# Kernel optimization log

Measured on AMD Instinct MI355X. Metric: run time of the kernel, lower is better.

Reference implementation:

```python
import jax, jax.numpy as jnp
import numpy as np

B = 4096          # number of graphs
NPG = 148         # nodes per graph (fixed by ReadOut(num_nodes=148))
N = B * NPG       # total nodes = 606208
EPG = 592         # edges per graph (~avg degree 4: RNA backbone + base pairs)
E = B * EPG       # total edges = 2424832


def setup_inputs() -> dict:
    key = jax.random.key(0)
    ks = jax.random.split(key, 10)
    x = jax.random.normal(ks[0], (N, 4), jnp.float32)
    # edges confined within each graph via per-graph node offsets
    src = jax.random.randint(ks[1], (E,), 0, NPG, dtype=jnp.int32)
    dst = jax.random.randint(ks[2], (E,), 0, NPG, dtype=jnp.int32)
    offs = jnp.repeat(jnp.arange(B, dtype=jnp.int32) * NPG, EPG)
    edge_index = jnp.stack([src + offs, dst + offs], axis=0)
    batch = jnp.repeat(jnp.arange(B, dtype=jnp.int32), NPG)
    # GCNConv weights (glorot-ish) and biases: 4->16->32->64
    def glorot(k, fi, fo):
        return jax.random.normal(k, (fi, fo), jnp.float32) * np.sqrt(2.0 / (fi + fo)).astype(np.float32)
    W1 = glorot(ks[3], 4, 16); b1 = jnp.zeros((16,), jnp.float32)
    W2 = glorot(ks[4], 16, 32); b2 = jnp.zeros((32,), jnp.float32)
    W3 = glorot(ks[5], 32, 64); b3 = jnp.zeros((64,), jnp.float32)
    return {"x": x, "edge_index": edge_index, "batch": batch,
            "W1": W1, "b1": b1, "W2": W2, "b2": b2, "W3": W3, "b3": b3}


def gcn_conv(x, src, dst, W, b, n):
    """PyG GCNConv: x' = D^{-1/2}(A+I)D^{-1/2} (x W) + b."""
    h = x @ W                                   # [n, out]
    loop = jnp.arange(n, dtype=src.dtype)       # self loops
    s = jnp.concatenate([src, loop])
    d = jnp.concatenate([dst, loop])
    deg = jax.ops.segment_sum(jnp.ones_like(s, h.dtype), d, num_segments=n)
    dis = jnp.where(deg > 0, jax.lax.rsqrt(jnp.maximum(deg, 1e-12)), 0.0)
    norm = dis[s] * dis[d]                      # [n_edges_with_loops]
    msg = h[s] * norm[:, None]                  # gather + normalize
    return jax.ops.segment_sum(msg, d, num_segments=n) + b


def reference(x, edge_index, batch, W1, b1, W2, b2, W3, b3):
    src, dst = edge_index[0], edge_index[1]
    n = x.shape[0]
    # Dropout(p=0.1) is identity at inference time
    h = jax.nn.relu(gcn_conv(x, src, dst, W1, b1, n))
    h = jax.nn.relu(gcn_conv(h, src, dst, W2, b2, n))
    h = jax.nn.relu(gcn_conv(h, src, dst, W3, b3, n))
    # to_dense_batch with max_num_nodes=148: every graph has exactly 148 nodes
    # and `batch` is sorted block-constant, so dense batching == reshape.
    dense = h.reshape(B, NPG, h.shape[-1])      # [B, 148, 64]
    return dense.reshape(B, -1)                 # Flatten -> [B, 9472]
```

## Files before the change

### kernel.cpp

```cpp
#include <hip/hip_runtime.h>

#define NPG 148
#define EPG 592
#define NTHR 256
#define SA   40
#define MT   10

typedef _Float16 h8 __attribute__((ext_vector_type(8)));
typedef _Float16 h4 __attribute__((ext_vector_type(4)));
typedef float    f4 __attribute__((ext_vector_type(4)));

__device__ __forceinline__ float f16bits_to_f32(unsigned short u) {
    return (float)__builtin_bit_cast(_Float16, u);
}


template<int Fi, int Fo, int KC, int NTN, int MAXJ, int WROW, int BOFF, bool LAST>
__device__ __forceinline__ void layer(int t,
    _Float16* __restrict__ A16, const _Float16* __restrict__ Wt,
    const _Float16* __restrict__ s_bh, const unsigned int* __restrict__ s_csr,
    const unsigned short* __restrict__ s_row, const unsigned short* __restrict__ s_dis,
    float* __restrict__ gout)
{
    float a[KC][8];
    if (t < NPG) {
        const float dd = f16bits_to_f32(s_dis[t]);
        const char* selfb = reinterpret_cast<const char*>(A16) + t * (SA * 2);
        #pragma unroll
        for (int kc = 0; kc < KC; ++kc) {
            const h8 hv = *reinterpret_cast<const h8*>(selfb + kc * 16);
            #pragma unroll
            for (int u = 0; u < 8; ++u) a[kc][u] = dd * (float)hv[u];
        }
        int e  = s_row[t];
        const int e1 = s_row[t + 1];
        unsigned int pk = (e < e1) ? s_csr[e] : 0u;
        while (e < e1) {
            const unsigned int pknext = (e + 1 < e1) ? s_csr[e + 1] : 0u;
            const char* mb = reinterpret_cast<const char*>(A16) + (pk & 0xffffu);
            const float ds = f16bits_to_f32((unsigned short)(pk >> 16));
            #pragma unroll
            for (int kc = 0; kc < KC; ++kc) {
                const h8 m = *reinterpret_cast<const h8*>(mb + kc * 16);
                #pragma unroll
                for (int u = 0; u < 8; ++u) a[kc][u] = fmaf((float)m[u], ds, a[kc][u]);
            }
            pk = pknext;
            ++e;
        }
        #pragma unroll
        for (int kc = 0; kc < KC; ++kc)
            #pragma unroll
            for (int u = 0; u < 8; ++u) a[kc][u] *= dd;
    }
    __syncthreads();
    if (t < NPG) {
        char* selfb = reinterpret_cast<char*>(A16) + t * (SA * 2);
        #pragma unroll
        for (int kc = 0; kc < KC; ++kc) {
            h8 pv;
            #pragma unroll
            for (int u = 0; u < 8; ++u) pv[u] = (_Float16)a[kc][u];
            *reinterpret_cast<h8*>(selfb + kc * 16) = pv;
        }
    }
    __syncthreads();

    const int w   = t >> 6;
    const int l16 = t & 15;
    const int q   = (t >> 4) & 3;
    h8 af[MAXJ], bf[MAXJ];
    #pragma unroll
    for (int j = 0; j < MAXJ; ++j) {
        const int idx = w + 4 * j;
        if (idx < MT * NTN) {
            const int mt = idx / NTN, nt = idx % NTN;
            af[j] = *reinterpret_cast<const h8*>(&A16[(mt * 16 + l16) * SA + q * 8]);
            bf[j] = *reinterpret_cast<const h8*>(&Wt[(WROW + nt * 16 + l16) * SA + q * 8]);
        }
    }
    __syncthreads();
    #pragma unroll
    for (int j = 0; j < MAXJ; ++j) {
        const int idx = w + 4 * j;
        if (idx < MT * NTN) {
            const int mt = idx / NTN, nt = idx % NTN;
            f4 acc = {0.f, 0.f, 0.f, 0.f};
            acc = __builtin_amdgcn_mfma_f32_16x16x32_f16(af[j], bf[j], acc, 0, 0, 0);
            const int col  = nt * 16 + l16;
            const float bias = (float)s_bh[BOFF + col];
            #pragma unroll
            for (int rr = 0; rr < 4; ++rr) {
                const float v = fmaxf(acc[rr] + bias, 0.f);
                const int row = mt * 16 + q * 4 + rr;
                if (LAST) {
                    if (row < NPG) gout[row * 64 + col] = v;
                } else {
                    A16[row * SA + col] = (_Float16)v;
                }
            }
        }
    }
    if (!LAST) __syncthreads();
}

__global__ __launch_bounds__(256, 6)
void gcn_fused(const float* __restrict__ x,
               const int* __restrict__ esrc, const int* __restrict__ edst,
               const float* __restrict__ W1, const float* __restrict__ b1,
               const float* __restrict__ W2, const float* __restrict__ b2,
               const float* __restrict__ W3, const float* __restrict__ b3,
               float* __restrict__ out)
{
    __shared__ __align__(16) _Float16 A16[160 * SA];
    __shared__ __align__(16) _Float16 Wt[112 * SA];
    __shared__ _Float16 s_bh[112];
    __shared__ unsigned int s_csr[EPG];
    __shared__ unsigned short s_row[152];
    __shared__ unsigned short s_dis[NPG];
    __shared__ int s_cnt[NPG], s_cnt2[NPG];

    int* s_edge = reinterpret_cast<int*>(Wt);

    const int t  = threadIdx.x;
    const int g  = blockIdx.x;
    const int be = g * EPG;
    const int bn = g * NPG;

    if (t < NPG) { s_cnt[t] = 0; s_cnt2[t] = 0; }
    for (int e = t; e < EPG; e += NTHR) {
        const int s = esrc[be + e] - bn;
        const int d = edst[be + e] - bn;
        s_edge[e] = s | (d << 8);
    }
    __syncthreads();

    for (int e = t; e < EPG; e += NTHR)
        atomicAdd(&s_cnt[((unsigned)s_edge[e]) >> 8], 1);
    __syncthreads();

    if (t < NPG) {
        const float disf = rsqrtf((float)(s_cnt[t] + 1));
        s_dis[t] = __builtin_bit_cast(unsigned short, (_Float16)disf);
    }
    if (t < 64) {
        const int lane = t;
        int v0 = s_cnt[lane];
        int v1 = s_cnt[64 + lane];
        int v2 = (128 + lane < NPG) ? s_cnt[128 + lane] : 0;
        #pragma unroll
        for (int off = 1; off < 64; off <<= 1) {
            const int u0 = __shfl_up(v0, off);
            const int u1 = __shfl_up(v1, off);
            const int u2 = __shfl_up(v2, off);
            if (lane >= off) { v0 += u0; v1 += u1; v2 += u2; }
        }
        const int t0 = __shfl(v0, 63);
        const int t1 = __shfl(v1, 63);
        v1 += t0;
        v2 += t0 + t1;
        if (lane == 0) s_row[0] = 0;
        s_row[1 + lane]  = (unsigned short)v0;
        s_row[65 + lane] = (unsigned short)v1;
        if (128 + lane < NPG) s_row[129 + lane] = (unsigned short)v2;
    }
    __syncthreads();

    for (int e = t; e < EPG; e += NTHR) {
        const int pk = s_edge[e];
        const int s  = pk & 0xFF;
        const int d  = (unsigned)pk >> 8;
        const int pos = (int)s_row[d] + atomicAdd(&s_cnt2[d], 1);
        s_csr[pos] = (unsigned int)(s * (SA * 2)) | ((unsigned int)s_dis[s] << 16);
    }
    __syncthreads();

    for (int i = t; i < 160 * SA / 8; i += NTHR) reinterpret_cast<f4*>(A16)[i] = f4{0.f, 0.f, 0.f, 0.f};
    for (int i = t; i < 112 * SA / 8; i += NTHR) reinterpret_cast<f4*>(Wt)[i]  = f4{0.f, 0.f, 0.f, 0.f};
    __syncthreads();
    for (int i = t; i < 64;   i += NTHR) Wt[(i & 15) * SA + (i >> 4)]        = (_Float16)W1[i];
    for (int i = t; i < 512;  i += NTHR) Wt[(16 + (i & 31)) * SA + (i >> 5)] = (_Float16)W2[i];
    for (int i = t; i < 2048; i += NTHR) Wt[(48 + (i & 63)) * SA + (i >> 6)] = (_Float16)W3[i];
    if (t < 16)       s_bh[t] = (_Float16)b1[t];
    else if (t < 48)  s_bh[t] = (_Float16)b2[t - 16];
    else if (t < 112) s_bh[t] = (_Float16)b3[t - 48];
    if (t < NPG) {
        const float4 xv = reinterpret_cast<const float4*>(x)[bn + t];
        h4 p; p[0] = (_Float16)xv.x; p[1] = (_Float16)xv.y; p[2] = (_Float16)xv.z; p[3] = (_Float16)xv.w;
        *reinterpret_cast<h4*>(&A16[t * SA]) = p;
    }
    __syncthreads();

    float* gout = out + (size_t)bn * 64;
    layer< 4, 16,  1,  1,   3,    0,   0, false>(t, A16, Wt, s_bh, s_csr, s_row, s_dis, gout);
    layer<16, 32,  2,  2,   5,   16,  16, false>(t, A16, Wt, s_bh, s_csr, s_row, s_dis, gout);
    layer<32, 64,  4,  4,  10,   48,  48, true >(t, A16, Wt, s_bh, s_csr, s_row, s_dis, gout);
}

extern "C" void kernel_launch(void* const* d_in, const int* in_sizes, int n_in,
                              void* d_out, int out_size, void* d_ws, size_t ws_size,
                              hipStream_t stream)
{
    const float* x  = (const float*)d_in[0];
    const int*   ei = (const int*)d_in[1];
    const float* W1 = (const float*)d_in[3];
    const float* b1 = (const float*)d_in[4];
    const float* W2 = (const float*)d_in[5];
    const float* b2 = (const float*)d_in[6];
    const float* W3 = (const float*)d_in[7];
    const float* b3 = (const float*)d_in[8];
    float* out = (float*)d_out;

    const int N = in_sizes[0] / 4;
    const int B = N / NPG;
    const int E = in_sizes[1] / 2;

    gcn_fused<<<B, NTHR, 0, stream>>>(x, ei, ei + E, W1, b1, W2, b2, W3, b3, out);
}
```

Before: 64.96 us.

## Split per-graph CSR construction into a separate setup kernel via workspace

Moves degree counting, the prefix scan, the normalization factors and the CSR edge sort out of the fused kernel into a new setup kernel. The setup kernel handles one graph per wavefront and writes packed CSR entries and row/degree metadata to the workspace. The main kernel then just loads the precomputed CSR and metadata into LDS, which shortens its serial prologue and cuts its LDS use, aiming at higher occupancy. It also shrinks the activation row stride from 40 to 36 halves, with a separate 40-half stride for weights, and vectorizes the W3 load. The trade-offs are an extra launch and an extra global write and read of the CSR data, and the 72-byte activation rows leave the 16-byte LDS vector loads only 8-byte aligned.

```diff
diff --git a/kernel.cpp b/kernel.cpp
--- a/kernel.cpp
+++ b/kernel.cpp
@@ -3,28 +3,120 @@
 #define NPG 148
 #define EPG 592
 #define NTHR 256
-#define SA   40
+#define SA   36
+#define SW   40
 #define MT   10
+#define MPG  149
 
 typedef _Float16 h8 __attribute__((ext_vector_type(8)));
 typedef _Float16 h4 __attribute__((ext_vector_type(4)));
 typedef float    f4 __attribute__((ext_vector_type(4)));
-
-__device__ __forceinline__ float f16bits_to_f32(unsigned short u) {
+typedef unsigned int u32;
+
+__device__ __forceinline__ float f16b(unsigned short u) {
     return (float)__builtin_bit_cast(_Float16, u);
 }
-
+__device__ __forceinline__ u32 f16u(float v) {
+    return (u32)__builtin_bit_cast(unsigned short, (_Float16)v);
+}
+
+__global__ __launch_bounds__(256, 8)
+void gcn_setup(const int* __restrict__ esrc, const int* __restrict__ edst,
+               u32* __restrict__ csr_g, u32* __restrict__ meta_g)
+{
+    __shared__ int cnt[4][160];
+    __shared__ u32 rows[4][148];
+    __shared__ u32 cbuf[4][EPG];
+
+    const int t  = threadIdx.x;
+    const int wv = t >> 6;
+    const int l  = t & 63;
+    const int g  = blockIdx.x * 4 + wv;
+    const int be = g * EPG;
+    const int bn = g * NPG;
+
+    u32 ep[10];
+    #pragma unroll
+    for (int k = 0; k < 10; ++k) {
+        const int e = l + k * 64;
+        ep[k] = 0xffffffffu;
+        if (e < EPG) {
+            const int s = esrc[be + e] - bn;
+            const int d = edst[be + e] - bn;
+            ep[k] = (u32)(s | (d << 8));
+        }
+    }
+    cnt[wv][l] = 0; cnt[wv][64 + l] = 0;
+    if (l < 32) cnt[wv][128 + l] = 0;
+    __syncthreads();
+
+    #pragma unroll
+    for (int k = 0; k < 10; ++k)
+        if (ep[k] != 0xffffffffu) atomicAdd(&cnt[wv][(ep[k] >> 8) & 0xff], 1);
+    __syncthreads();
+
+    const int c0 = cnt[wv][l];
+    const int c1 = cnt[wv][64 + l];
+    const int c2 = (l < 20) ? cnt[wv][128 + l] : 0;
+    int v0 = c0, v1 = c1, v2 = c2;
+    #pragma unroll
+    for (int off = 1; off < 64; off <<= 1) {
+        const int u0 = __shfl_up(v0, off);
+        const int u1 = __shfl_up(v1, off);
+        const int u2 = __shfl_up(v2, off);
+        if (l >= off) { v0 += u0; v1 += u1; v2 += u2; }
+    }
+    const int t0 = __shfl(v0, 63);
+    const int t1 = __shfl(v1, 63);
+    const int r0 = v0 - c0;
+    const int r1 = v1 - c1 + t0;
+    const int r2 = v2 - c2 + t0 + t1;
+    const u32 m0 = ((u32)r0 << 16) | f16u(rsqrtf((float)(c0 + 1)));
+    const u32 m1 = ((u32)r1 << 16) | f16u(rsqrtf((float)(c1 + 1)));
+    const u32 m2 = ((u32)r2 << 16) | f16u(rsqrtf((float)(c2 + 1)));
+    rows[wv][l] = m0;
+    rows[wv][64 + l] = m1;
+    if (l < 20) rows[wv][128 + l] = m2;
+    const size_t gm = (size_t)g * MPG;
+    meta_g[gm + l] = m0;
+    meta_g[gm + 64 + l] = m1;
+    if (l < 20) meta_g[gm + 128 + l] = m2;
+    if (l == 0) meta_g[gm + 148] = (u32)EPG << 16;
+
+    __syncthreads();
+    cnt[wv][l] = 0; cnt[wv][64 + l] = 0;
+    if (l < 32) cnt[wv][128 + l] = 0;
+    __syncthreads();
+
+    #pragma unroll
+    for (int k = 0; k < 10; ++k)
+        if (ep[k] != 0xffffffffu) {
+            const int s = ep[k] & 0xff;
+            const int d = (ep[k] >> 8) & 0xff;
+            const int pos = (int)(rows[wv][d] >> 16) + atomicAdd(&cnt[wv][d], 1);
+            cbuf[wv][pos] = (u32)(s * (SA * 2)) | ((rows[wv][s] & 0xffffu) << 16);
+        }
+    __syncthreads();
+
+    u32* cg = csr_g + (size_t)g * EPG;
+    #pragma unroll
+    for (int k = 0; k < 10; ++k) {
+        const int e = l + k * 64;
+        if (e < EPG) cg[e] = cbuf[wv][e];
+    }
+}
 
 template<int Fi, int Fo, int KC, int NTN, int MAXJ, int WROW, int BOFF, bool LAST>
 __device__ __forceinline__ void layer(int t,
     _Float16* __restrict__ A16, const _Float16* __restrict__ Wt,
-    const _Float16* __restrict__ s_bh, const unsigned int* __restrict__ s_csr,
-    const unsigned short* __restrict__ s_row, const unsigned short* __restrict__ s_dis,
-    float* __restrict__ gout)
+    const _Float16* __restrict__ s_bh, const u32* __restrict__ s_csr,
+    const u32* __restrict__ s_meta, float* __restrict__ gout)
 {
     float a[KC][8];
     if (t < NPG) {
-        const float dd = f16bits_to_f32(s_dis[t]);
+        const u32 me  = s_meta[t];
+        const u32 me2 = s_meta[t + 1];
+        const float dd = f16b((unsigned short)(me & 0xffffu));
         const char* selfb = reinterpret_cast<const char*>(A16) + t * (SA * 2);
         #pragma unroll
         for (int kc = 0; kc < KC; ++kc) {
@@ -32,20 +124,20 @@
             #pragma unroll
             for (int u = 0; u < 8; ++u) a[kc][u] = dd * (float)hv[u];
         }
-        int e  = s_row[t];
-        const int e1 = s_row[t + 1];
-        unsigned int pk = (e < e1) ? s_csr[e] : 0u;
+        int e  = (int)(me >> 16);
+        const int e1 = (int)(me2 >> 16);
+        u32 pk = (e < e1) ? s_csr[e] : 0u;
         while (e < e1) {
-            const unsigned int pknext = (e + 1 < e1) ? s_csr[e + 1] : 0u;
+            const u32 pn = (e + 1 < e1) ? s_csr[e + 1] : 0u;
             const char* mb = reinterpret_cast<const char*>(A16) + (pk & 0xffffu);
-            const float ds = f16bits_to_f32((unsigned short)(pk >> 16));
+            const float ds = f16b((unsigned short)(pk >> 16));
             #pragma unroll
             for (int kc = 0; kc < KC; ++kc) {
                 const h8 m = *reinterpret_cast<const h8*>(mb + kc * 16);
                 #pragma unroll
                 for (int u = 0; u < 8; ++u) a[kc][u] = fmaf((float)m[u], ds, a[kc][u]);
             }
-            pk = pknext;
+            pk = pn;
             ++e;
         }
         #pragma unroll
@@ -76,7 +168,7 @@
         if (idx < MT * NTN) {
             const int mt = idx / NTN, nt = idx % NTN;
             af[j] = *reinterpret_cast<const h8*>(&A16[(mt * 16 + l16) * SA + q * 8]);
-            bf[j] = *reinterpret_cast<const h8*>(&Wt[(WROW + nt * 16 + l16) * SA + q * 8]);
+            bf[j] = *reinterpret_cast<const h8*>(&Wt[(WROW + nt * 16 + l16) * SW + q * 8]);
         }
     }
     __syncthreads();
@@ -104,83 +196,48 @@
     if (!LAST) __syncthreads();
 }
 
-__global__ __launch_bounds__(256, 6)
-void gcn_fused(const float* __restrict__ x,
-               const int* __restrict__ esrc, const int* __restrict__ edst,
-               const float* __restrict__ W1, const float* __restrict__ b1,
-               const float* __restrict__ W2, const float* __restrict__ b2,
-               const float* __restrict__ W3, const float* __restrict__ b3,
-               float* __restrict__ out)
+__global__ __launch_bounds__(NTHR, 6)
+void gcn_main(const float* __restrict__ x,
+              const u32* __restrict__ csr_g, const u32* __restrict__ meta_g,
+              const float* __restrict__ W1, const float* __restrict__ b1,
+              const float* __restrict__ W2, const float* __restrict__ b2,
+              const float* __restrict__ W3, const float* __restrict__ b3,
+              float* __restrict__ out)
 {
     __shared__ __align__(16) _Float16 A16[160 * SA];
-    __shared__ __align__(16) _Float16 Wt[112 * SA];
+    __shared__ __align__(16) _Float16 Wt[112 * SW];
     __shared__ _Float16 s_bh[112];
-    __shared__ unsigned int s_csr[EPG];
-    __shared__ unsigned short s_row[152];
-    __shared__ unsigned short s_dis[NPG];
-    __shared__ int s_cnt[NPG], s_cnt2[NPG];
-
-    int* s_edge = reinterpret_cast<int*>(Wt);
-
-    const int t  = threadIdx.x;
-    const int g  = blockIdx.x;
-    const int be = g * EPG;
+    __shared__ u32 s_csr[EPG];
+    __shared__ u32 s_meta[MPG + 3];
+
+    const int t = threadIdx.x;
+    const int g = blockIdx.x;
     const int bn = g * NPG;
 
-    if (t < NPG) { s_cnt[t] = 0; s_cnt2[t] = 0; }
-    for (int e = t; e < EPG; e += NTHR) {
-        const int s = esrc[be + e] - bn;
-        const int d = edst[be + e] - bn;
-        s_edge[e] = s | (d << 8);
-    }
-    __syncthreads();
-
-    for (int e = t; e < EPG; e += NTHR)
-        atomicAdd(&s_cnt[((unsigned)s_edge[e]) >> 8], 1);
-    __syncthreads();
-
-    if (t < NPG) {
-        const float disf = rsqrtf((float)(s_cnt[t] + 1));
-        s_dis[t] = __builtin_bit_cast(unsigned short, (_Float16)disf);
-    }
-    if (t < 64) {
-        const int lane = t;
-        int v0 = s_cnt[lane];
-        int v1 = s_cnt[64 + lane];
-        int v2 = (128 + lane < NPG) ? s_cnt[128 + lane] : 0;
-        #pragma unroll
-        for (int off = 1; off < 64; off <<= 1) {
-            const int u0 = __shfl_up(v0, off);
-            const int u1 = __shfl_up(v1, off);
-            const int u2 = __shfl_up(v2, off);
-            if (lane >= off) { v0 += u0; v1 += u1; v2 += u2; }
-        }
-        const int t0 = __shfl(v0, 63);
-        const int t1 = __shfl(v1, 63);
-        v1 += t0;
-        v2 += t0 + t1;
-        if (lane == 0) s_row[0] = 0;
-        s_row[1 + lane]  = (unsigned short)v0;
-        s_row[65 + lane] = (unsigned short)v1;
-        if (128 + lane < NPG) s_row[129 + lane] = (unsigned short)v2;
-    }
-    __syncthreads();
-
-    for (int e = t; e < EPG; e += NTHR) {
-        const int pk = s_edge[e];
-        const int s  = pk & 0xFF;
-        const int d  = (unsigned)pk >> 8;
-        const int pos = (int)s_row[d] + atomicAdd(&s_cnt2[d], 1);
-        s_csr[pos] = (unsigned int)(s * (SA * 2)) | ((unsigned int)s_dis[s] << 16);
-    }
-    __syncthreads();
-
-    for (int i = t; i < 160 * SA / 8; i += NTHR) reinterpret_cast<f4*>(A16)[i] = f4{0.f, 0.f, 0.f, 0.f};
-    for (int i = t; i < 112 * SA / 8; i += NTHR) reinterpret_cast<f4*>(Wt)[i]  = f4{0.f, 0.f, 0.f, 0.f};
-    __syncthreads();
-    for (int i = t; i < 64;   i += NTHR) Wt[(i & 15) * SA + (i >> 4)]        = (_Float16)W1[i];
-    for (int i = t; i < 512;  i += NTHR) Wt[(16 + (i & 31)) * SA + (i >> 5)] = (_Float16)W2[i];
-    for (int i = t; i < 2048; i += NTHR) Wt[(48 + (i & 63)) * SA + (i >> 6)] = (_Float16)W3[i];
+    for (int i = t; i < 160 * SA / 8; i += NTHR)
+        reinterpret_cast<f4*>(A16)[i] = f4{0.f, 0.f, 0.f, 0.f};
+    for (int i = t; i < 112 * SW / 8; i += NTHR)
+        reinterpret_cast<f4*>(Wt)[i] = f4{0.f, 0.f, 0.f, 0.f};
+    __syncthreads();
+
+    {
+        const u32* cg = csr_g + (size_t)g * EPG;
+        for (int i = t; i < EPG; i += NTHR) s_csr[i] = cg[i];
+        const u32* mg = meta_g + (size_t)g * MPG;
+        if (t < MPG) s_meta[t] = mg[t];
+    }
+    if (t < 64) Wt[(t & 15) * SW + (t >> 4)] = (_Float16)W1[t];
+    for (int i = t; i < 512; i += NTHR)
+        Wt[(16 + (i & 31)) * SW + (i >> 5)] = (_Float16)W2[i];
+    for (int i = t; i < 512; i += NTHR) {
+        const f4 wv = reinterpret_cast<const f4*>(W3)[i];
+        const int j = 4 * i;
+        const int k = j >> 6;
+        const int c = j & 63;
+        #pragma unroll
+        for (int u = 0; u < 4; ++u)
+            Wt[(48 + c + u) * SW + k] = (_Float16)wv[u];
+    }
     if (t < 16)       s_bh[t] = (_Float16)b1[t];
     else if (t < 48)  s_bh[t] = (_Float16)b2[t - 16];
     else if (t < 112) s_bh[t] = (_Float16)b3[t - 48];
@@ -192,9 +249,9 @@
     __syncthreads();
 
     float* gout = out + (size_t)bn * 64;
-    layer< 4, 16,  1,  1,   3,    0,   0, false>(t, A16, Wt, s_bh, s_csr, s_row, s_dis, gout);
-    layer<16, 32,  2,  2,   5,   16,  16, false>(t, A16, Wt, s_bh, s_csr, s_row, s_dis, gout);
-    layer<32, 64,  4,  4,  10,   48,  48, true >(t, A16, Wt, s_bh, s_csr, s_row, s_dis, gout);
+    layer< 4, 16,  1,  1,   3,    0,   0, false>(t, A16, Wt, s_bh, s_csr, s_meta, gout);
+    layer<16, 32,  2,  2,   5,   16,  16, false>(t, A16, Wt, s_bh, s_csr, s_meta, gout);
+    layer<32, 64,  4,  4,  10,   48,  48, true >(t, A16, Wt, s_bh, s_csr, s_meta, gout);
 }
 
 extern "C" void kernel_launch(void* const* d_in, const int* in_sizes, int n_in,
@@ -215,5 +272,9 @@
     const int B = N / NPG;
     const int E = in_sizes[1] / 2;
 
-    gcn_fused<<<B, NTHR, 0, stream>>>(x, ei, ei + E, W1, b1, W2, b2, W3, b3, out);
-}
+    u32* csr_g  = (u32*)d_ws;
+    u32* meta_g = csr_g + (size_t)B * EPG;
+
+    gcn_setup<<<B / 4, NTHR, 0, stream>>>(ei, ei + E, csr_g, meta_g);
+    gcn_main <<<B,     NTHR, 0, stream>>>(x, csr_g, meta_g, W1, b1, W2, b2, W3, b3, out);
+}
```

Measured after the change: 116.4 us. 1.79x slower.

## Pre-scale node features by D^-1/2 and aggregate in packed fp16

Applied to the files above, without the earlier changes.

Node features are now multiplied by their own inverse-sqrt degree when they are written: on the initial x load and in each non-final layer's MFMA epilogue. Edge aggregation then becomes a plain packed-fp16 vector add with no per-edge scale and no fp32 conversions. The activation row stride shrinks from 40 to 36 halves, while the weights keep a separate 40-half stride, and the x global load is issued earlier to overlap with edge setup. Risks are lost accuracy from accumulating in fp16 and 16-byte LDS vector accesses on a 72-byte row stride that is no longer 16-byte aligned.

```diff
diff --git a/kernel.cpp b/kernel.cpp
--- a/kernel.cpp
+++ b/kernel.cpp
@@ -3,14 +3,16 @@
 #define NPG 148
 #define EPG 592
 #define NTHR 256
-#define SA   40
+#define SA   36
+#define SW   40
 #define MT   10
 
 typedef _Float16 h8 __attribute__((ext_vector_type(8)));
 typedef _Float16 h4 __attribute__((ext_vector_type(4)));
 typedef float    f4 __attribute__((ext_vector_type(4)));
-
-__device__ __forceinline__ float f16bits_to_f32(unsigned short u) {
+typedef unsigned int u32;
+
+__device__ __forceinline__ float f16b(unsigned short u) {
     return (float)__builtin_bit_cast(_Float16, u);
 }
 
@@ -18,51 +20,41 @@
 template<int Fi, int Fo, int KC, int NTN, int MAXJ, int WROW, int BOFF, bool LAST>
 __device__ __forceinline__ void layer(int t,
     _Float16* __restrict__ A16, const _Float16* __restrict__ Wt,
-    const _Float16* __restrict__ s_bh, const unsigned int* __restrict__ s_csr,
+    const _Float16* __restrict__ s_bh, const u32* __restrict__ s_csr,
     const unsigned short* __restrict__ s_row, const unsigned short* __restrict__ s_dis,
     float* __restrict__ gout)
 {
-    float a[KC][8];
-    if (t < NPG) {
-        const float dd = f16bits_to_f32(s_dis[t]);
+    h8 a[KC];
+    if (t < NPG) {
         const char* selfb = reinterpret_cast<const char*>(A16) + t * (SA * 2);
         #pragma unroll
-        for (int kc = 0; kc < KC; ++kc) {
-            const h8 hv = *reinterpret_cast<const h8*>(selfb + kc * 16);
-            #pragma unroll
-            for (int u = 0; u < 8; ++u) a[kc][u] = dd * (float)hv[u];
-        }
+        for (int kc = 0; kc < KC; ++kc)
+            a[kc] = *reinterpret_cast<const h8*>(selfb + kc * 16);
         int e  = s_row[t];
         const int e1 = s_row[t + 1];
-        unsigned int pk = (e < e1) ? s_csr[e] : 0u;
+        u32 pk = (e < e1) ? s_csr[e] : 0u;
         while (e < e1) {
-            const unsigned int pknext = (e + 1 < e1) ? s_csr[e + 1] : 0u;
+            const u32 pn = (e + 1 < e1) ? s_csr[e + 1] : 0u;
             const char* mb = reinterpret_cast<const char*>(A16) + (pk & 0xffffu);
-            const float ds = f16bits_to_f32((unsigned short)(pk >> 16));
             #pragma unroll
-            for (int kc = 0; kc < KC; ++kc) {
-                const h8 m = *reinterpret_cast<const h8*>(mb + kc * 16);
-                #pragma unroll
-                for (int u = 0; u < 8; ++u) a[kc][u] = fmaf((float)m[u], ds, a[kc][u]);
-            }
-            pk = pknext;
+            for (int kc = 0; kc < KC; ++kc)
+                a[kc] += *reinterpret_cast<const h8*>(mb + kc * 16);
+            pk = pn;
             ++e;
         }
+        const _Float16 ddh = __builtin_bit_cast(_Float16, s_dis[t]);
+        h8 ddv;
+        #pragma unroll
+        for (int u = 0; u < 8; ++u) ddv[u] = ddh;
+        #pragma unroll
+        for (int kc = 0; kc < KC; ++kc) a[kc] *= ddv;
+    }
+    __syncthreads();
+    if (t < NPG) {
+        char* selfb = reinterpret_cast<char*>(A16) + t * (SA * 2);
         #pragma unroll
         for (int kc = 0; kc < KC; ++kc)
-            #pragma unroll
-            for (int u = 0; u < 8; ++u) a[kc][u] *= dd;
-    }
-    __syncthreads();
-    if (t < NPG) {
-        char* selfb = reinterpret_cast<char*>(A16) + t * (SA * 2);
-        #pragma unroll
-        for (int kc = 0; kc < KC; ++kc) {
-            h8 pv;
-            #pragma unroll
-            for (int u = 0; u < 8; ++u) pv[u] = (_Float16)a[kc][u];
-            *reinterpret_cast<h8*>(selfb + kc * 16) = pv;
-        }
+            *reinterpret_cast<h8*>(selfb + kc * 16) = a[kc];
     }
     __syncthreads();
 
@@ -76,7 +68,7 @@
         if (idx < MT * NTN) {
             const int mt = idx / NTN, nt = idx % NTN;
             af[j] = *reinterpret_cast<const h8*>(&A16[(mt * 16 + l16) * SA + q * 8]);
-            bf[j] = *reinterpret_cast<const h8*>(&Wt[(WROW + nt * 16 + l16) * SA + q * 8]);
+            bf[j] = *reinterpret_cast<const h8*>(&Wt[(WROW + nt * 16 + l16) * SW + q * 8]);
         }
     }
     __syncthreads();
@@ -89,14 +81,16 @@
             acc = __builtin_amdgcn_mfma_f32_16x16x32_f16(af[j], bf[j], acc, 0, 0, 0);
             const int col  = nt * 16 + l16;
             const float bias = (float)s_bh[BOFF + col];
+            const int r0 = mt * 16 + q * 4;
             #pragma unroll
             for (int rr = 0; rr < 4; ++rr) {
+                const int row = r0 + rr;
                 const float v = fmaxf(acc[rr] + bias, 0.f);
-                const int row = mt * 16 + q * 4 + rr;
                 if (LAST) {
                     if (row < NPG) gout[row * 64 + col] = v;
                 } else {
-                    A16[row * SA + col] = (_Float16)v;
+                    const float dsr = (row < NPG) ? f16b(s_dis[row]) : 0.f;
+                    A16[row * SA + col] = (_Float16)(v * dsr);
                 }
             }
         }
@@ -104,7 +98,7 @@
     if (!LAST) __syncthreads();
 }
 
-__global__ __launch_bounds__(256, 6)
+__global__ __launch_bounds__(NTHR, 6)
 void gcn_fused(const float* __restrict__ x,
                const int* __restrict__ esrc, const int* __restrict__ edst,
                const float* __restrict__ W1, const float* __restrict__ b1,
@@ -113,9 +107,9 @@
                float* __restrict__ out)
 {
     __shared__ __align__(16) _Float16 A16[160 * SA];
-    __shared__ __align__(16) _Float16 Wt[112 * SA];
+    __shared__ __align__(16) _Float16 Wt[112 * SW];
     __shared__ _Float16 s_bh[112];
-    __shared__ unsigned int s_csr[EPG];
+    __shared__ u32 s_csr[EPG];
     __shared__ unsigned short s_row[152];
     __shared__ unsigned short s_dis[NPG];
     __shared__ int s_cnt[NPG], s_cnt2[NPG];
@@ -128,6 +122,8 @@
     const int bn = g * NPG;
 
     if (t < NPG) { s_cnt[t] = 0; s_cnt2[t] = 0; }
+    float4 xv;
+    if (t < NPG) xv = reinterpret_cast<const float4*>(x)[bn + t];
     for (int e = t; e < EPG; e += NTHR) {
         const int s = esrc[be + e] - bn;
         const int d = edst[be + e] - bn;
@@ -171,22 +167,24 @@
         const int s  = pk & 0xFF;
         const int d  = (unsigned)pk >> 8;
         const int pos = (int)s_row[d] + atomicAdd(&s_cnt2[d], 1);
-        s_csr[pos] = (unsigned int)(s * (SA * 2)) | ((unsigned int)s_dis[s] << 16);
+        s_csr[pos] = (u32)(s * (SA * 2)) | ((u32)s_dis[s] << 16);
     }
     __syncthreads();
 
     for (int i = t; i < 160 * SA / 8; i += NTHR) reinterpret_cast<f4*>(A16)[i] = f4{0.f, 0.f, 0.f, 0.f};
-    for (int i = t; i < 112 * SA / 8; i += NTHR) reinterpret_cast<f4*>(Wt)[i]  = f4{0.f, 0.f, 0.f, 0.f};
-    __syncthreads();
-    for (int i = t; i < 64;   i += NTHR) Wt[(i & 15) * SA + (i >> 4)]        = (_Float16)W1[i];
-    for (int i = t; i < 512;  i += NTHR) Wt[(16 + (i & 31)) * SA + (i >> 5)] = (_Float16)W2[i];
-    for (int i = t; i < 2048; i += NTHR) Wt[(48 + (i & 63)) * SA + (i >> 6)] = (_Float16)W3[i];
+    for (int i = t; i < 112 * SW / 8; i += NTHR) reinterpret_cast<f4*>(Wt)[i]  = f4{0.f, 0.f, 0.f, 0.f};
+    __syncthreads();
+    for (int i = t; i < 64;   i += NTHR) Wt[(i & 15) * SW + (i >> 4)]        = (_Float16)W1[i];
+    for (int i = t; i < 512;  i += NTHR) Wt[(16 + (i & 31)) * SW + (i >> 5)] = (_Float16)W2[i];
+    for (int i = t; i < 2048; i += NTHR) Wt[(48 + (i & 63)) * SW + (i >> 6)] = (_Float16)W3[i];
     if (t < 16)       s_bh[t] = (_Float16)b1[t];
     else if (t < 48)  s_bh[t] = (_Float16)b2[t - 16];
     else if (t < 112) s_bh[t] = (_Float16)b3[t - 48];
     if (t < NPG) {
-        const float4 xv = reinterpret_cast<const float4*>(x)[bn + t];
-        h4 p; p[0] = (_Float16)xv.x; p[1] = (_Float16)xv.y; p[2] = (_Float16)xv.z; p[3] = (_Float16)xv.w;
+        const float dsf = f16b(s_dis[t]);
+        h4 p;
+        p[0] = (_Float16)(xv.x * dsf); p[1] = (_Float16)(xv.y * dsf);
+        p[2] = (_Float16)(xv.z * dsf); p[3] = (_Float16)(xv.w * dsf);
         *reinterpret_cast<h4*>(&A16[t * SA]) = p;
     }
     __syncthreads();
```

New measurement: 110.2 us. 69.6% more time.
